# Performance work log

Hardware: AMD Instinct MI355X
Metric: run time of the kernel (lower is better)

## Reference

```python
import jax, jax.numpy as jnp
import numpy as np


def setup_inputs() -> dict:
    key = jax.random.key(0)
    ks = jax.random.split(key, 6)
    B, N, D, C = 16, 4096, 1024, 4
    bags = jax.random.normal(ks[0], (B, N, D), dtype=jnp.float32)
    query = jax.random.normal(ks[1], (D,), dtype=jnp.float32)
    W1 = jax.random.normal(ks[2], (3 * D, 512), dtype=jnp.float32) * 0.02
    b1 = jax.random.normal(ks[3], (512,), dtype=jnp.float32) * 0.02
    W2 = jax.random.normal(ks[4], (512, C), dtype=jnp.float32) * 0.02
    b2 = jax.random.normal(ks[5], (C,), dtype=jnp.float32) * 0.02
    return {"bags": bags, "query": query, "W1": W1, "b1": b1, "W2": W2, "b2": b2}


def reference(bags, query, W1, b1, W2, b2):
    # bags: [B, N, D] instance features (frozen feat_extractor output)
    mean_pool = jnp.mean(bags, axis=1)                     # [B, D]
    max_pool = jnp.max(bags, axis=1)                       # [B, D]
    # attention pooling: softmax over instances of <bag_i, query>
    scores = jax.nn.softmax(jnp.einsum('bnd,d->bn', bags, query), axis=1)  # [B, N]
    attn_pool = jnp.einsum('bn,bnd->bd', scores, bags)     # [B, D]
    x = jnp.concatenate([mean_pool, max_pool, attn_pool], axis=-1)  # [B, 3D]
    x = x @ W1 + b1
    x = x @ W2 + b2
    return x
```

## Files before the change

### kernel.cpp

```cpp
#include <hip/hip_runtime.h>
#include <math.h>

#define BNUM 16
#define NNUM 4096
#define DNUM 1024
#define CNUM 4
#define HNUM 512

#define SCH   64
#define ROWS  (NNUM / SCH)
#define RPW   (ROWS / 4)

#define PSTRIDE 3080
#define NPART   (BNUM * SCH)
#define XOFF    ((size_t)NPART * PSTRIDE)
#define WOFF    (XOFF + (size_t)BNUM * 3 * DNUM)
#define BIASOFF (WOFF + (size_t)3 * DNUM * 4)

#define NEG_INF (-__builtin_inff())

__global__ __launch_bounds__(256) void k_mainpass(const float* __restrict__ bags,
                                                  const float* __restrict__ query,
                                                  float* __restrict__ ws) {
    const int chunk = blockIdx.x;
    const int b     = blockIdx.y;
    const int tid   = threadIdx.x;
    const int wave  = tid >> 6;
    const int lane  = tid & 63;

    const float4* q4 = (const float4*)query;
    float4 q[4];
#pragma unroll
    for (int s = 0; s < 4; ++s) q[s] = q4[s * 64 + lane];

    float4 sum[4], mx[4], acc[4];
#pragma unroll
    for (int s = 0; s < 4; ++s) {
        sum[s] = make_float4(0.f, 0.f, 0.f, 0.f);
        acc[s] = make_float4(0.f, 0.f, 0.f, 0.f);
        mx[s]  = make_float4(NEG_INF, NEG_INF, NEG_INF, NEG_INF);
    }
    float m = NEG_INF, l = 0.f;

    const int n0 = chunk * ROWS + wave * RPW;
    const float4* base = (const float4*)(bags + (size_t)b * NNUM * DNUM);

    for (int r = 0; r < RPW; r += 2) {
        const float4* rowA = base + (size_t)(n0 + r) * (DNUM / 4);
        const float4* rowB = rowA + (DNUM / 4);
        float4 va[4], vb[4];
#pragma unroll
        for (int s = 0; s < 4; ++s) va[s] = rowA[s * 64 + lane];
#pragma unroll
        for (int s = 0; s < 4; ++s) vb[s] = rowB[s * 64 + lane];

        float pa = 0.f, pb = 0.f;
#pragma unroll
        for (int s = 0; s < 4; ++s) {
            pa += va[s].x * q[s].x + va[s].y * q[s].y + va[s].z * q[s].z + va[s].w * q[s].w;
            pb += vb[s].x * q[s].x + vb[s].y * q[s].y + vb[s].z * q[s].z + vb[s].w * q[s].w;
        }
#pragma unroll
        for (int off = 32; off; off >>= 1) {
            pa += __shfl_xor(pa, off, 64);
            pb += __shfl_xor(pb, off, 64);
        }

        const float mnew = fmaxf(m, fmaxf(pa, pb));
        if (mnew > m) {
            const float alpha = __expf(m - mnew);
            l *= alpha;
#pragma unroll
            for (int s = 0; s < 4; ++s) {
                acc[s].x *= alpha; acc[s].y *= alpha;
                acc[s].z *= alpha; acc[s].w *= alpha;
            }
            m = mnew;
        }
        const float wa = __expf(pa - m);
        const float wb = __expf(pb - m);
        l += wa + wb;

#pragma unroll
        for (int s = 0; s < 4; ++s) {
            sum[s].x += va[s].x + vb[s].x;
            sum[s].y += va[s].y + vb[s].y;
            sum[s].z += va[s].z + vb[s].z;
            sum[s].w += va[s].w + vb[s].w;
            mx[s].x = fmaxf(mx[s].x, fmaxf(va[s].x, vb[s].x));
            mx[s].y = fmaxf(mx[s].y, fmaxf(va[s].y, vb[s].y));
            mx[s].z = fmaxf(mx[s].z, fmaxf(va[s].z, vb[s].z));
            mx[s].w = fmaxf(mx[s].w, fmaxf(va[s].w, vb[s].w));
            acc[s].x += wa * va[s].x + wb * vb[s].x;
            acc[s].y += wa * va[s].y + wb * vb[s].y;
            acc[s].z += wa * va[s].z + wb * vb[s].z;
            acc[s].w += wa * va[s].w + wb * vb[s].w;
        }
    }

    __shared__ float buf[4][DNUM];
    __shared__ float sm[4], sl[4];
    if (lane == 0) { sm[wave] = m; sl[wave] = l; }

    float* wsp = ws + (size_t)(b * SCH + chunk) * PSTRIDE;

#pragma unroll
    for (int s = 0; s < 4; ++s) ((float4*)(&buf[wave][s * 256]))[lane] = sum[s];
    __syncthreads();
    {
        float4 a0 = ((float4*)buf[0])[tid];
        float4 a1 = ((float4*)buf[1])[tid];
        float4 a2 = ((float4*)buf[2])[tid];
        float4 a3 = ((float4*)buf[3])[tid];
        float4 r;
        r.x = a0.x + a1.x + a2.x + a3.x;
        r.y = a0.y + a1.y + a2.y + a3.y;
        r.z = a0.z + a1.z + a2.z + a3.z;
        r.w = a0.w + a1.w + a2.w + a3.w;
        ((float4*)wsp)[tid] = r;
    }
    __syncthreads();

#pragma unroll
    for (int s = 0; s < 4; ++s) ((float4*)(&buf[wave][s * 256]))[lane] = mx[s];
    __syncthreads();
    {
        float4 a0 = ((float4*)buf[0])[tid];
        float4 a1 = ((float4*)buf[1])[tid];
        float4 a2 = ((float4*)buf[2])[tid];
        float4 a3 = ((float4*)buf[3])[tid];
        float4 r;
        r.x = fmaxf(fmaxf(a0.x, a1.x), fmaxf(a2.x, a3.x));
        r.y = fmaxf(fmaxf(a0.y, a1.y), fmaxf(a2.y, a3.y));
        r.z = fmaxf(fmaxf(a0.z, a1.z), fmaxf(a2.z, a3.z));
        r.w = fmaxf(fmaxf(a0.w, a1.w), fmaxf(a2.w, a3.w));
        ((float4*)(wsp + 1024))[tid] = r;
    }
    __syncthreads();

#pragma unroll
    for (int s = 0; s < 4; ++s) ((float4*)(&buf[wave][s * 256]))[lane] = acc[s];
    __syncthreads();
    {
        const float m0 = sm[0], m1 = sm[1], m2 = sm[2], m3 = sm[3];
        const float mb = fmaxf(fmaxf(m0, m1), fmaxf(m2, m3));
        const float e0 = __expf(m0 - mb), e1 = __expf(m1 - mb);
        const float e2 = __expf(m2 - mb), e3 = __expf(m3 - mb);
        float4 a0 = ((float4*)buf[0])[tid];
        float4 a1 = ((float4*)buf[1])[tid];
        float4 a2 = ((float4*)buf[2])[tid];
        float4 a3 = ((float4*)buf[3])[tid];
        float4 r;
        r.x = a0.x * e0 + a1.x * e1 + a2.x * e2 + a3.x * e3;
        r.y = a0.y * e0 + a1.y * e1 + a2.y * e2 + a3.y * e3;
        r.z = a0.z * e0 + a1.z * e1 + a2.z * e2 + a3.z * e3;
        r.w = a0.w * e0 + a1.w * e1 + a2.w * e2 + a3.w * e3;
        ((float4*)(wsp + 2048))[tid] = r;
        if (tid == 0) {
            wsp[3072] = mb;
            wsp[3073] = sl[0] * e0 + sl[1] * e1 + sl[2] * e2 + sl[3] * e3;
        }
    }
}

__global__ __launch_bounds__(256) void k_weff(const float* __restrict__ W1,
                                              const float* __restrict__ W2,
                                              const float* __restrict__ b1,
                                              const float* __restrict__ b2,
                                              float* __restrict__ ws) {
    const int tid  = threadIdx.x;
    const int wave = tid >> 6, lane = tid & 63;
    const float4* w2 = (const float4*)W2;

    if (blockIdx.x < 768) {
        const int k = blockIdx.x * 4 + wave;
        const float* r = W1 + (size_t)k * HNUM;
        float a0 = 0.f, a1 = 0.f, a2 = 0.f, a3 = 0.f;
#pragma unroll
        for (int t = 0; t < 8; ++t) {
            const int j = lane * 8 + t;
            const float  wv = r[j];
            const float4 w  = w2[j];
            a0 += wv * w.x; a1 += wv * w.y; a2 += wv * w.z; a3 += wv * w.w;
        }
#pragma unroll
        for (int off = 32; off; off >>= 1) {
            a0 += __shfl_xor(a0, off, 64);
            a1 += __shfl_xor(a1, off, 64);
            a2 += __shfl_xor(a2, off, 64);
            a3 += __shfl_xor(a3, off, 64);
        }
        if (lane == 0)
            ((float4*)(ws + WOFF))[k] = make_float4(a0, a1, a2, a3);
    } else if (wave == 0) {
        float a0 = 0.f, a1 = 0.f, a2 = 0.f, a3 = 0.f;
#pragma unroll
        for (int t = 0; t < 8; ++t) {
            const int j = lane * 8 + t;
            const float  bv = b1[j];
            const float4 w  = w2[j];
            a0 += bv * w.x; a1 += bv * w.y; a2 += bv * w.z; a3 += bv * w.w;
        }
#pragma unroll
        for (int off = 32; off; off >>= 1) {
            a0 += __shfl_xor(a0, off, 64);
            a1 += __shfl_xor(a1, off, 64);
            a2 += __shfl_xor(a2, off, 64);
            a3 += __shfl_xor(a3, off, 64);
        }
        if (lane == 0) {
            float* bias = ws + BIASOFF;
            bias[0] = a0 + b2[0];
            bias[1] = a1 + b2[1];
            bias[2] = a2 + b2[2];
            bias[3] = a3 + b2[3];
        }
    }
}

__global__ __launch_bounds__(256) void k_finish(const float* __restrict__ ws,
                                                float* __restrict__ out) {
    const int b    = blockIdx.x;
    const int tid  = threadIdx.x;
    const int wave = tid >> 6, lane = tid & 63;

    __shared__ float eS[SCH];
    __shared__ float lbS;
    __shared__ float red[4][4];

    const float* pb = ws + (size_t)b * SCH * PSTRIDE;

    if (wave == 0) {
        const float* p = pb + (size_t)lane * PSTRIDE;
        const float mlane = p[3072];
        const float llane = p[3073];
        float mb = mlane;
#pragma unroll
        for (int off = 32; off; off >>= 1) mb = fmaxf(mb, __shfl_xor(mb, off, 64));
        const float e = __expf(mlane - mb);
        float lb = llane * e;
#pragma unroll
        for (int off = 32; off; off >>= 1) lb += __shfl_xor(lb, off, 64);
        eS[lane] = e;
        if (lane == 0) lbS = lb;
    }
    __syncthreads();
    const float inv_lb = 1.f / lbS;

    float4 s  = make_float4(0.f, 0.f, 0.f, 0.f);
    float4 a  = make_float4(0.f, 0.f, 0.f, 0.f);
    float4 mxv = make_float4(NEG_INF, NEG_INF, NEG_INF, NEG_INF);
    for (int c = 0; c < SCH; ++c) {
        const float* p = pb + (size_t)c * PSTRIDE;
        const float4 sv = ((const float4*)p)[tid];
        const float4 mv = ((const float4*)(p + 1024))[tid];
        const float4 av = ((const float4*)(p + 2048))[tid];
        const float e = eS[c];
        s.x += sv.x; s.y += sv.y; s.z += sv.z; s.w += sv.w;
        mxv.x = fmaxf(mxv.x, mv.x); mxv.y = fmaxf(mxv.y, mv.y);
        mxv.z = fmaxf(mxv.z, mv.z); mxv.w = fmaxf(mxv.w, mv.w);
        a.x += e * av.x; a.y += e * av.y; a.z += e * av.z; a.w += e * av.w;
    }

    const float4* weff = (const float4*)(ws + WOFF);
    float c0 = 0.f, c1 = 0.f, c2 = 0.f, c3 = 0.f;
    const float scm = 1.f / NNUM;
    const float xm[4] = { s.x * scm, s.y * scm, s.z * scm, s.w * scm };
    const float xx[4] = { mxv.x, mxv.y, mxv.z, mxv.w };
    const float xa[4] = { a.x * inv_lb, a.y * inv_lb, a.z * inv_lb, a.w * inv_lb };
#pragma unroll
    for (int k = 0; k < 4; ++k) {
        const float4 w = weff[tid * 4 + k];
        c0 += xm[k] * w.x; c1 += xm[k] * w.y; c2 += xm[k] * w.z; c3 += xm[k] * w.w;
    }
#pragma unroll
    for (int k = 0; k < 4; ++k) {
        const float4 w = weff[DNUM + tid * 4 + k];
        c0 += xx[k] * w.x; c1 += xx[k] * w.y; c2 += xx[k] * w.z; c3 += xx[k] * w.w;
    }
#pragma unroll
    for (int k = 0; k < 4; ++k) {
        const float4 w = weff[2 * DNUM + tid * 4 + k];
        c0 += xa[k] * w.x; c1 += xa[k] * w.y; c2 += xa[k] * w.z; c3 += xa[k] * w.w;
    }
#pragma unroll
    for (int off = 32; off; off >>= 1) {
        c0 += __shfl_xor(c0, off, 64);
        c1 += __shfl_xor(c1, off, 64);
        c2 += __shfl_xor(c2, off, 64);
        c3 += __shfl_xor(c3, off, 64);
    }
    if (lane == 0) { red[wave][0] = c0; red[wave][1] = c1; red[wave][2] = c2; red[wave][3] = c3; }
    __syncthreads();
    if (tid < 4) {
        const float* bias = ws + BIASOFF;
        out[b * 4 + tid] = red[0][tid] + red[1][tid] + red[2][tid] + red[3][tid] + bias[tid];
    }
}

extern "C" void kernel_launch(void* const* d_in, const int* in_sizes, int n_in,
                              void* d_out, int out_size, void* d_ws, size_t ws_size,
                              hipStream_t stream) {
    const float* bags  = (const float*)d_in[0];
    const float* query = (const float*)d_in[1];
    const float* W1    = (const float*)d_in[2];
    const float* b1    = (const float*)d_in[3];
    const float* W2    = (const float*)d_in[4];
    const float* b2    = (const float*)d_in[5];
    float* out = (float*)d_out;
    float* ws  = (float*)d_ws;

    k_weff    <<<769,             256, 0, stream>>>(W1, W2, b1, b2, ws);
    k_mainpass<<<dim3(SCH, BNUM), 256, 0, stream>>>(bags, query, ws);
    k_finish  <<<BNUM,            256, 0, stream>>>(ws, out);
}
```

Before: 393.3 us.

## Fuse weight-fold, main pass and finish into one kernel with atomic last-block reduction

New measurement: 609.1 us. 1.55x slower.

```diff
diff --git a/kernel.cpp b/kernel.cpp
--- a/kernel.cpp
+++ b/kernel.cpp
@@ -16,222 +16,236 @@
 #define XOFF    ((size_t)NPART * PSTRIDE)
 #define WOFF    (XOFF + (size_t)BNUM * 3 * DNUM)
 #define BIASOFF (WOFF + (size_t)3 * DNUM * 4)
+#define CTRWOFF (BIASOFF + 8)
+
+#define NWEFF   769
+#define NMAIN   (SCH * BNUM)
 
 #define NEG_INF (-__builtin_inff())
 
-__global__ __launch_bounds__(256) void k_mainpass(const float* __restrict__ bags,
+typedef float vf4 __attribute__((ext_vector_type(4)));
+
+__device__ __forceinline__ void load_pair(const vf4* rowA, int lane,
+                                          vf4 (&va)[4], vf4 (&vb)[4]) {
+    const vf4* rowB = rowA + (DNUM / 4);
+#pragma unroll
+    for (int s = 0; s < 4; ++s) va[s] = __builtin_nontemporal_load(rowA + s * 64 + lane);
+#pragma unroll
+    for (int s = 0; s < 4; ++s) vb[s] = __builtin_nontemporal_load(rowB + s * 64 + lane);
+}
+
+__device__ __forceinline__ void process_pair(const vf4 (&va)[4], const vf4 (&vb)[4],
+                                             const vf4 (&q)[4],
+                                             vf4 (&sum)[4], vf4 (&mx)[4], vf4 (&acc)[4],
+                                             float& m, float& l) {
+    float pa = 0.f, pb = 0.f;
+#pragma unroll
+    for (int s = 0; s < 4; ++s) {
+        pa += va[s].x * q[s].x + va[s].y * q[s].y + va[s].z * q[s].z + va[s].w * q[s].w;
+        pb += vb[s].x * q[s].x + vb[s].y * q[s].y + vb[s].z * q[s].z + vb[s].w * q[s].w;
+    }
+#pragma unroll
+    for (int off = 32; off; off >>= 1) {
+        pa += __shfl_xor(pa, off, 64);
+        pb += __shfl_xor(pb, off, 64);
+    }
+    const float mnew = fmaxf(m, fmaxf(pa, pb));
+    if (mnew > m) {
+        const float alpha = __expf(m - mnew);
+        l *= alpha;
+#pragma unroll
+        for (int s = 0; s < 4; ++s) acc[s] *= alpha;
+        m = mnew;
+    }
+    const float wa = __expf(pa - m);
+    const float wb = __expf(pb - m);
+    l += wa + wb;
+#pragma unroll
+    for (int s = 0; s < 4; ++s) {
+        sum[s] += va[s] + vb[s];
+        mx[s].x = fmaxf(mx[s].x, fmaxf(va[s].x, vb[s].x));
+        mx[s].y = fmaxf(mx[s].y, fmaxf(va[s].y, vb[s].y));
+        mx[s].z = fmaxf(mx[s].z, fmaxf(va[s].z, vb[s].z));
+        mx[s].w = fmaxf(mx[s].w, fmaxf(va[s].w, vb[s].w));
+        acc[s] += wa * va[s] + wb * vb[s];
+    }
+}
+
+__global__ __launch_bounds__(256, 3) void k_fused(const float* __restrict__ bags,
                                                   const float* __restrict__ query,
-                                                  float* __restrict__ ws) {
-    const int chunk = blockIdx.x;
-    const int b     = blockIdx.y;
-    const int tid   = threadIdx.x;
-    const int wave  = tid >> 6;
-    const int lane  = tid & 63;
-
-    const float4* q4 = (const float4*)query;
-    float4 q[4];
-#pragma unroll
-    for (int s = 0; s < 4; ++s) q[s] = q4[s * 64 + lane];
-
-    float4 sum[4], mx[4], acc[4];
-#pragma unroll
-    for (int s = 0; s < 4; ++s) {
-        sum[s] = make_float4(0.f, 0.f, 0.f, 0.f);
-        acc[s] = make_float4(0.f, 0.f, 0.f, 0.f);
-        mx[s]  = make_float4(NEG_INF, NEG_INF, NEG_INF, NEG_INF);
-    }
-    float m = NEG_INF, l = 0.f;
-
-    const int n0 = chunk * ROWS + wave * RPW;
-    const float4* base = (const float4*)(bags + (size_t)b * NNUM * DNUM);
-
-    for (int r = 0; r < RPW; r += 2) {
-        const float4* rowA = base + (size_t)(n0 + r) * (DNUM / 4);
-        const float4* rowB = rowA + (DNUM / 4);
-        float4 va[4], vb[4];
-#pragma unroll
-        for (int s = 0; s < 4; ++s) va[s] = rowA[s * 64 + lane];
-#pragma unroll
-        for (int s = 0; s < 4; ++s) vb[s] = rowB[s * 64 + lane];
-
-        float pa = 0.f, pb = 0.f;
-#pragma unroll
-        for (int s = 0; s < 4; ++s) {
-            pa += va[s].x * q[s].x + va[s].y * q[s].y + va[s].z * q[s].z + va[s].w * q[s].w;
-            pb += vb[s].x * q[s].x + vb[s].y * q[s].y + vb[s].z * q[s].z + vb[s].w * q[s].w;
-        }
-#pragma unroll
-        for (int off = 32; off; off >>= 1) {
-            pa += __shfl_xor(pa, off, 64);
-            pb += __shfl_xor(pb, off, 64);
-        }
-
-        const float mnew = fmaxf(m, fmaxf(pa, pb));
-        if (mnew > m) {
-            const float alpha = __expf(m - mnew);
-            l *= alpha;
-#pragma unroll
-            for (int s = 0; s < 4; ++s) {
-                acc[s].x *= alpha; acc[s].y *= alpha;
-                acc[s].z *= alpha; acc[s].w *= alpha;
-            }
-            m = mnew;
-        }
-        const float wa = __expf(pa - m);
-        const float wb = __expf(pb - m);
-        l += wa + wb;
-
-#pragma unroll
-        for (int s = 0; s < 4; ++s) {
-            sum[s].x += va[s].x + vb[s].x;
-            sum[s].y += va[s].y + vb[s].y;
-            sum[s].z += va[s].z + vb[s].z;
-            sum[s].w += va[s].w + vb[s].w;
-            mx[s].x = fmaxf(mx[s].x, fmaxf(va[s].x, vb[s].x));
-            mx[s].y = fmaxf(mx[s].y, fmaxf(va[s].y, vb[s].y));
-            mx[s].z = fmaxf(mx[s].z, fmaxf(va[s].z, vb[s].z));
-            mx[s].w = fmaxf(mx[s].w, fmaxf(va[s].w, vb[s].w));
-            acc[s].x += wa * va[s].x + wb * vb[s].x;
-            acc[s].y += wa * va[s].y + wb * vb[s].y;
-            acc[s].z += wa * va[s].z + wb * vb[s].z;
-            acc[s].w += wa * va[s].w + wb * vb[s].w;
-        }
-    }
+                                                  const float* __restrict__ W1,
+                                                  const float* __restrict__ b1,
+                                                  const float* __restrict__ W2,
+                                                  const float* __restrict__ b2,
+                                                  float* __restrict__ ws,
+                                                  float* __restrict__ out) {
+    const int tid  = threadIdx.x;
+    const int wave = tid >> 6;
+    const int lane = tid & 63;
+    unsigned int* ctrs = (unsigned int*)(ws + CTRWOFF);
 
     __shared__ float buf[4][DNUM];
     __shared__ float sm[4], sl[4];
+    __shared__ int   isFin;
+    __shared__ float eS[SCH];
+    __shared__ float lbS;
+    __shared__ float red[4][4];
+
+    if (blockIdx.x < NWEFF) {
+        const vf4* w2 = (const vf4*)W2;
+        if (blockIdx.x < 768) {
+            const int k = blockIdx.x * 4 + wave;
+            const float* r = W1 + (size_t)k * HNUM;
+            float a0 = 0.f, a1 = 0.f, a2 = 0.f, a3 = 0.f;
+#pragma unroll
+            for (int t = 0; t < 8; ++t) {
+                const int j = lane * 8 + t;
+                const float wv = r[j];
+                const vf4   w  = w2[j];
+                a0 += wv * w.x; a1 += wv * w.y; a2 += wv * w.z; a3 += wv * w.w;
+            }
+#pragma unroll
+            for (int off = 32; off; off >>= 1) {
+                a0 += __shfl_xor(a0, off, 64);
+                a1 += __shfl_xor(a1, off, 64);
+                a2 += __shfl_xor(a2, off, 64);
+                a3 += __shfl_xor(a3, off, 64);
+            }
+            if (lane == 0) {
+                vf4 rv; rv.x = a0; rv.y = a1; rv.z = a2; rv.w = a3;
+                ((vf4*)(ws + WOFF))[k] = rv;
+            }
+        } else if (wave == 0) {
+            float a0 = 0.f, a1 = 0.f, a2 = 0.f, a3 = 0.f;
+#pragma unroll
+            for (int t = 0; t < 8; ++t) {
+                const int j = lane * 8 + t;
+                const float bv = b1[j];
+                const vf4   w  = w2[j];
+                a0 += bv * w.x; a1 += bv * w.y; a2 += bv * w.z; a3 += bv * w.w;
+            }
+#pragma unroll
+            for (int off = 32; off; off >>= 1) {
+                a0 += __shfl_xor(a0, off, 64);
+                a1 += __shfl_xor(a1, off, 64);
+                a2 += __shfl_xor(a2, off, 64);
+                a3 += __shfl_xor(a3, off, 64);
+            }
+            if (lane == 0) {
+                float* bias = ws + BIASOFF;
+                bias[0] = a0 + b2[0]; bias[1] = a1 + b2[1];
+                bias[2] = a2 + b2[2]; bias[3] = a3 + b2[3];
+            }
+        }
+        __threadfence();
+        __syncthreads();
+        if (tid == 0) atomicAdd(&ctrs[0], 1u);
+        return;
+    }
+
+    const int v     = blockIdx.x - NWEFF;
+    const int chunk = v & (SCH - 1);
+    const int b     = v >> 6;
+
+    const vf4* q4 = (const vf4*)query;
+    vf4 q[4];
+#pragma unroll
+    for (int s = 0; s < 4; ++s) q[s] = q4[s * 64 + lane];
+
+    vf4 sum[4], mx[4], acc[4];
+#pragma unroll
+    for (int s = 0; s < 4; ++s) {
+        sum[s] = (vf4)0.f;
+        acc[s] = (vf4)0.f;
+        mx[s]  = (vf4)NEG_INF;
+    }
+    float m = NEG_INF, l = 0.f;
+
+    const int n0 = chunk * ROWS + wave * RPW;
+    const vf4* base = (const vf4*)(bags + (size_t)b * NNUM * DNUM);
+
+    vf4 va[4], vb[4], na[4], nb[4];
+    load_pair(base + (size_t)n0 * (DNUM / 4), lane, va, vb);
+    for (int r = 0; r < RPW; r += 4) {
+        load_pair(base + (size_t)(n0 + r + 2) * (DNUM / 4), lane, na, nb);
+        process_pair(va, vb, q, sum, mx, acc, m, l);
+        if (r + 4 < RPW)
+            load_pair(base + (size_t)(n0 + r + 4) * (DNUM / 4), lane, va, vb);
+        process_pair(na, nb, q, sum, mx, acc, m, l);
+    }
+
     if (lane == 0) { sm[wave] = m; sl[wave] = l; }
 
     float* wsp = ws + (size_t)(b * SCH + chunk) * PSTRIDE;
 
 #pragma unroll
-    for (int s = 0; s < 4; ++s) ((float4*)(&buf[wave][s * 256]))[lane] = sum[s];
+    for (int s = 0; s < 4; ++s) ((vf4*)(&buf[wave][s * 256]))[lane] = sum[s];
     __syncthreads();
     {
-        float4 a0 = ((float4*)buf[0])[tid];
-        float4 a1 = ((float4*)buf[1])[tid];
-        float4 a2 = ((float4*)buf[2])[tid];
-        float4 a3 = ((float4*)buf[3])[tid];
-        float4 r;
-        r.x = a0.x + a1.x + a2.x + a3.x;
-        r.y = a0.y + a1.y + a2.y + a3.y;
-        r.z = a0.z + a1.z + a2.z + a3.z;
-        r.w = a0.w + a1.w + a2.w + a3.w;
-        ((float4*)wsp)[tid] = r;
-    }
-    __syncthreads();
-
-#pragma unroll
-    for (int s = 0; s < 4; ++s) ((float4*)(&buf[wave][s * 256]))[lane] = mx[s];
+        vf4 a0 = ((vf4*)buf[0])[tid];
+        vf4 a1 = ((vf4*)buf[1])[tid];
+        vf4 a2 = ((vf4*)buf[2])[tid];
+        vf4 a3 = ((vf4*)buf[3])[tid];
+        ((vf4*)wsp)[tid] = a0 + a1 + a2 + a3;
+    }
+    __syncthreads();
+
+#pragma unroll
+    for (int s = 0; s < 4; ++s) ((vf4*)(&buf[wave][s * 256]))[lane] = mx[s];
     __syncthreads();
     {
-        float4 a0 = ((float4*)buf[0])[tid];
-        float4 a1 = ((float4*)buf[1])[tid];
-        float4 a2 = ((float4*)buf[2])[tid];
-        float4 a3 = ((float4*)buf[3])[tid];
-        float4 r;
+        vf4 a0 = ((vf4*)buf[0])[tid];
+        vf4 a1 = ((vf4*)buf[1])[tid];
+        vf4 a2 = ((vf4*)buf[2])[tid];
+        vf4 a3 = ((vf4*)buf[3])[tid];
+        vf4 r;
         r.x = fmaxf(fmaxf(a0.x, a1.x), fmaxf(a2.x, a3.x));
         r.y = fmaxf(fmaxf(a0.y, a1.y), fmaxf(a2.y, a3.y));
         r.z = fmaxf(fmaxf(a0.z, a1.z), fmaxf(a2.z, a3.z));
         r.w = fmaxf(fmaxf(a0.w, a1.w), fmaxf(a2.w, a3.w));
-        ((float4*)(wsp + 1024))[tid] = r;
-    }
-    __syncthreads();
-
-#pragma unroll
-    for (int s = 0; s < 4; ++s) ((float4*)(&buf[wave][s * 256]))[lane] = acc[s];
+        ((vf4*)(wsp + 1024))[tid] = r;
+    }
+    __syncthreads();
+
+#pragma unroll
+    for (int s = 0; s < 4; ++s) ((vf4*)(&buf[wave][s * 256]))[lane] = acc[s];
     __syncthreads();
     {
         const float m0 = sm[0], m1 = sm[1], m2 = sm[2], m3 = sm[3];
         const float mb = fmaxf(fmaxf(m0, m1), fmaxf(m2, m3));
         const float e0 = __expf(m0 - mb), e1 = __expf(m1 - mb);
         const float e2 = __expf(m2 - mb), e3 = __expf(m3 - mb);
-        float4 a0 = ((float4*)buf[0])[tid];
-        float4 a1 = ((float4*)buf[1])[tid];
-        float4 a2 = ((float4*)buf[2])[tid];
-        float4 a3 = ((float4*)buf[3])[tid];
-        float4 r;
-        r.x = a0.x * e0 + a1.x * e1 + a2.x * e2 + a3.x * e3;
-        r.y = a0.y * e0 + a1.y * e1 + a2.y * e2 + a3.y * e3;
-        r.z = a0.z * e0 + a1.z * e1 + a2.z * e2 + a3.z * e3;
-        r.w = a0.w * e0 + a1.w * e1 + a2.w * e2 + a3.w * e3;
-        ((float4*)(wsp + 2048))[tid] = r;
+        vf4 a0 = ((vf4*)buf[0])[tid];
+        vf4 a1 = ((vf4*)buf[1])[tid];
+        vf4 a2 = ((vf4*)buf[2])[tid];
+        vf4 a3 = ((vf4*)buf[3])[tid];
+        ((vf4*)(wsp + 2048))[tid] = a0 * e0 + a1 * e1 + a2 * e2 + a3 * e3;
         if (tid == 0) {
             wsp[3072] = mb;
             wsp[3073] = sl[0] * e0 + sl[1] * e1 + sl[2] * e2 + sl[3] * e3;
         }
     }
-}
-
-__global__ __launch_bounds__(256) void k_weff(const float* __restrict__ W1,
-                                              const float* __restrict__ W2,
-                                              const float* __restrict__ b1,
-                                              const float* __restrict__ b2,
-                                              float* __restrict__ ws) {
-    const int tid  = threadIdx.x;
-    const int wave = tid >> 6, lane = tid & 63;
-    const float4* w2 = (const float4*)W2;
-
-    if (blockIdx.x < 768) {
-        const int k = blockIdx.x * 4 + wave;
-        const float* r = W1 + (size_t)k * HNUM;
-        float a0 = 0.f, a1 = 0.f, a2 = 0.f, a3 = 0.f;
-#pragma unroll
-        for (int t = 0; t < 8; ++t) {
-            const int j = lane * 8 + t;
-            const float  wv = r[j];
-            const float4 w  = w2[j];
-            a0 += wv * w.x; a1 += wv * w.y; a2 += wv * w.z; a3 += wv * w.w;
+
+    __threadfence();
+    __syncthreads();
+    if (tid == 0) {
+        const unsigned old = atomicAdd(&ctrs[1 + b], 1u);
+        int fin = (old == SCH - 1);
+        if (fin) {
+            while (__hip_atomic_load(&ctrs[0], __ATOMIC_ACQUIRE,
+                                     __HIP_MEMORY_SCOPE_AGENT) < NWEFF)
+                __builtin_amdgcn_s_sleep(4);
         }
-#pragma unroll
-        for (int off = 32; off; off >>= 1) {
-            a0 += __shfl_xor(a0, off, 64);
-            a1 += __shfl_xor(a1, off, 64);
-            a2 += __shfl_xor(a2, off, 64);
-            a3 += __shfl_xor(a3, off, 64);
-        }
-        if (lane == 0)
-            ((float4*)(ws + WOFF))[k] = make_float4(a0, a1, a2, a3);
-    } else if (wave == 0) {
-        float a0 = 0.f, a1 = 0.f, a2 = 0.f, a3 = 0.f;
-#pragma unroll
-        for (int t = 0; t < 8; ++t) {
-            const int j = lane * 8 + t;
-            const float  bv = b1[j];
-            const float4 w  = w2[j];
-            a0 += bv * w.x; a1 += bv * w.y; a2 += bv * w.z; a3 += bv * w.w;
-        }
-#pragma unroll
-        for (int off = 32; off; off >>= 1) {
-            a0 += __shfl_xor(a0, off, 64);
-            a1 += __shfl_xor(a1, off, 64);
-            a2 += __shfl_xor(a2, off, 64);
-            a3 += __shfl_xor(a3, off, 64);
-        }
-        if (lane == 0) {
-            float* bias = ws + BIASOFF;
-            bias[0] = a0 + b2[0];
-            bias[1] = a1 + b2[1];
-            bias[2] = a2 + b2[2];
-            bias[3] = a3 + b2[3];
-        }
-    }
-}
-
-__global__ __launch_bounds__(256) void k_finish(const float* __restrict__ ws,
-                                                float* __restrict__ out) {
-    const int b    = blockIdx.x;
-    const int tid  = threadIdx.x;
-    const int wave = tid >> 6, lane = tid & 63;
-
-    __shared__ float eS[SCH];
-    __shared__ float lbS;
-    __shared__ float red[4][4];
-
-    const float* pb = ws + (size_t)b * SCH * PSTRIDE;
+        isFin = fin;
+    }
+    __syncthreads();
+    if (!isFin) return;
+    __threadfence();
+
+    const float* pbag = ws + (size_t)b * SCH * PSTRIDE;
 
     if (wave == 0) {
-        const float* p = pb + (size_t)lane * PSTRIDE;
+        const float* p = pbag + (size_t)lane * PSTRIDE;
         const float mlane = p[3072];
         const float llane = p[3073];
         float mb = mlane;
@@ -247,40 +261,39 @@
     __syncthreads();
     const float inv_lb = 1.f / lbS;
 
-    float4 s  = make_float4(0.f, 0.f, 0.f, 0.f);
-    float4 a  = make_float4(0.f, 0.f, 0.f, 0.f);
-    float4 mxv = make_float4(NEG_INF, NEG_INF, NEG_INF, NEG_INF);
+    vf4 fs = (vf4)0.f, fa = (vf4)0.f;
+    vf4 fm = (vf4)NEG_INF;
     for (int c = 0; c < SCH; ++c) {
-        const float* p = pb + (size_t)c * PSTRIDE;
-        const float4 sv = ((const float4*)p)[tid];
-        const float4 mv = ((const float4*)(p + 1024))[tid];
-        const float4 av = ((const float4*)(p + 2048))[tid];
+        const float* p = pbag + (size_t)c * PSTRIDE;
+        const vf4 sv = ((const vf4*)p)[tid];
+        const vf4 mv = ((const vf4*)(p + 1024))[tid];
+        const vf4 av = ((const vf4*)(p + 2048))[tid];
         const float e = eS[c];
-        s.x += sv.x; s.y += sv.y; s.z += sv.z; s.w += sv.w;
-        mxv.x = fmaxf(mxv.x, mv.x); mxv.y = fmaxf(mxv.y, mv.y);
-        mxv.z = fmaxf(mxv.z, mv.z); mxv.w = fmaxf(mxv.w, mv.w);
-        a.x += e * av.x; a.y += e * av.y; a.z += e * av.z; a.w += e * av.w;
-    }
-
-    const float4* weff = (const float4*)(ws + WOFF);
+        fs += sv;
+        fm.x = fmaxf(fm.x, mv.x); fm.y = fmaxf(fm.y, mv.y);
+        fm.z = fmaxf(fm.z, mv.z); fm.w = fmaxf(fm.w, mv.w);
+        fa += e * av;
+    }
+
+    const vf4* weff = (const vf4*)(ws + WOFF);
     float c0 = 0.f, c1 = 0.f, c2 = 0.f, c3 = 0.f;
     const float scm = 1.f / NNUM;
-    const float xm[4] = { s.x * scm, s.y * scm, s.z * scm, s.w * scm };
-    const float xx[4] = { mxv.x, mxv.y, mxv.z, mxv.w };
-    const float xa[4] = { a.x * inv_lb, a.y * inv_lb, a.z * inv_lb, a.w * inv_lb };
+    const float xm[4] = { fs.x * scm, fs.y * scm, fs.z * scm, fs.w * scm };
+    const float xx[4] = { fm.x, fm.y, fm.z, fm.w };
+    const float xa[4] = { fa.x * inv_lb, fa.y * inv_lb, fa.z * inv_lb, fa.w * inv_lb };
 #pragma unroll
     for (int k = 0; k < 4; ++k) {
-        const float4 w = weff[tid * 4 + k];
+        const vf4 w = weff[tid * 4 + k];
         c0 += xm[k] * w.x; c1 += xm[k] * w.y; c2 += xm[k] * w.z; c3 += xm[k] * w.w;
     }
 #pragma unroll
     for (int k = 0; k < 4; ++k) {
-        const float4 w = weff[DNUM + tid * 4 + k];
+        const vf4 w = weff[DNUM + tid * 4 + k];
         c0 += xx[k] * w.x; c1 += xx[k] * w.y; c2 += xx[k] * w.z; c3 += xx[k] * w.w;
     }
 #pragma unroll
     for (int k = 0; k < 4; ++k) {
-        const float4 w = weff[2 * DNUM + tid * 4 + k];
+        const vf4 w = weff[2 * DNUM + tid * 4 + k];
         c0 += xa[k] * w.x; c1 += xa[k] * w.y; c2 += xa[k] * w.z; c3 += xa[k] * w.w;
     }
 #pragma unroll
@@ -310,7 +323,6 @@
     float* out = (float*)d_out;
     float* ws  = (float*)d_ws;
 
-    k_weff    <<<769,             256, 0, stream>>>(W1, W2, b1, b2, ws);
-    k_mainpass<<<dim3(SCH, BNUM), 256, 0, stream>>>(bags, query, ws);
-    k_finish  <<<BNUM,            256, 0, stream>>>(ws, out);
+    hipMemsetAsync(ws + CTRWOFF, 0, 17 * sizeof(unsigned int), stream);
+    k_fused<<<NWEFF + NMAIN, 256, 0, stream>>>(bags, query, W1, b1, W2, b2, ws, out);
 }
```
